# Performance work log

Hardware: AMD Instinct MI355X
Metric: run time of the kernel (lower is better)

The kernel has to match this reference:

```python
import jax, jax.numpy as jnp
import numpy as np
import math

# config constants (match init_kwargs)
N_HEAD = 16
KNN_NUM = 4
MEM_FRAC = 4.0
BOOKKEEPING_FRAC = 0.0
RESID_ONLY = False
RESID_FOUND = 0.5   # set_resid_frac(resid_frac): found/current mix
RESID_CURR = 0.5
KNN_INFLUENCE = 1.0
NEG_INF = jnp.finfo(jnp.float32).min


def setup_inputs() -> dict:
    key = jax.random.key(0)
    k1, k2, k3, k4, k5 = jax.random.split(key, 5)
    B, T, C = 1, 2048, 1024
    H, d = N_HEAD, C // N_HEAD
    M = 8192  # per-head memory-store entries
    return {
        "x": jax.random.normal(k1, (B, T, C), jnp.float32),
        "c_attn_w": jax.random.normal(k2, (3 * C, C), jnp.float32) * 0.02,
        "c_proj_w": jax.random.normal(k3, (C, C), jnp.float32) * 0.02,
        "key_store": jax.random.normal(k4, (H, M, d), jnp.float32),
        "value_store": jax.random.normal(k5, (H, M, d), jnp.float32),
    }


def _knn_get(att, k, q, v, key_store, value_store):
    # att: (B,H,T,T), k/q/v: (B,H,T,d), stores: (H,M,d). B must be 1 (original
    # scatter offset i*t is only consistent for b==1).
    B, H, T, d = k.shape
    scale = 1.0 / math.sqrt(d)
    att_last = att[:, :, -1, :]                     # (B,H,T) last-query column
    # bookkeeping_frac == 0.0 -> skipped; mem_frac truthy -> threshold filter
    mask = att_last >= (1.0 / (MEM_FRAC * T))       # nonzero after zeroing

    # per-head flattened token lists, shape (H, N=B*T, d)
    kh = jnp.swapaxes(k, 0, 1).reshape(H, B * T, d)
    qh = jnp.swapaxes(q, 0, 1).reshape(H, B * T, d)
    vh = jnp.swapaxes(v, 0, 1).reshape(H, B * T, d)
    mask_h = jnp.swapaxes(mask, 0, 1).reshape(H, B * T)

    # exact L2 kNN (FAISS IndexFlatL2 equivalent): d2[h,n,m] = ||kh - ks||^2
    d2 = (jnp.sum(kh * kh, -1)[:, :, None]
          - 2.0 * jnp.einsum('hnd,hmd->hnm', kh, key_store)
          + jnp.sum(key_store * key_store, -1)[:, None, :])
    _, idx = jax.lax.top_k(-d2, KNN_NUM)            # (H,N,K) nearest indices

    h_ix = jnp.arange(H)[:, None, None]
    keys_found = key_store[h_ix, idx]               # (H,N,K,d)
    vals_found = value_store[h_ix, idx]
    keys_found = jnp.moveaxis(keys_found, 2, 0)     # (K,H,N,d)
    vals_found = jnp.moveaxis(vals_found, 2, 0)
    if not RESID_ONLY:
        keys_found = jnp.concatenate([kh[None], keys_found], axis=0)  # (K+1,H,N,d)
        vals_found = jnp.concatenate([vh[None], vals_found], axis=0)

    attf = jnp.einsum('khnd,hnd->khn', keys_found, qh) * scale
    attf = jnp.where(jnp.isnan(attf), NEG_INF, attf)
    attf = jax.nn.softmax(attf * KNN_INFLUENCE, axis=0)
    vals_new = jnp.einsum('khn,khnd->hnd', attf, vals_found)
    if RESID_FOUND > 0 or RESID_CURR > 0:
        vals_new = vals_new * RESID_FOUND + vh * RESID_CURR

    v_out = jnp.where(mask_h[..., None], vals_new, vh)   # scatter-equivalent
    return jnp.swapaxes(v_out.reshape(H, B, T, d), 0, 1)  # (B,H,T,d)


def reference(x, c_attn_w, c_proj_w, key_store, value_store):
    B, T, C = x.shape
    H, d = N_HEAD, C // N_HEAD
    qkv = x @ c_attn_w.T                             # (B,T,3C)
    q, k, v = jnp.split(qkv, 3, axis=2)
    q = jnp.swapaxes(q.reshape(B, T, H, d), 1, 2)    # (B,H,T,d)
    k = jnp.swapaxes(k.reshape(B, T, H, d), 1, 2)
    v = jnp.swapaxes(v.reshape(B, T, H, d), 1, 2)

    att = jnp.einsum('bhqd,bhkd->bhqk', q, k) * (1.0 / math.sqrt(d))
    causal = jnp.tril(jnp.ones((T, T), bool))
    att = jnp.where(causal, att, NEG_INF)
    att = jax.nn.softmax(att, axis=-1)

    # knn_get is @torch.no_grad() in the original -> stop_gradient
    v_new = jax.lax.stop_gradient(
        _knn_get(att, k, q, v, key_store, value_store))

    y = jnp.einsum('bhqk,bhkd->bhqd', att, v_new)
    y = jnp.swapaxes(y, 1, 2).reshape(B, T, C)
    return y @ c_proj_w.T
```

## Files before the change

kernel.cpp:

```cpp
#include <hip/hip_runtime.h>
#include <hip/hip_bf16.h>
#include <math.h>

#define TT 2048
#define CC 1024
#define HH 16
#define DDIM 64
#define MM 8192
#define C3 3072
#define SBIAS 256.0f

typedef __bf16 bf16x8 __attribute__((ext_vector_type(8)));
typedef float f32x4 __attribute__((ext_vector_type(4)));

__device__ __forceinline__ float waveReduceSum(float v) {
#pragma unroll
  for (int off = 32; off > 0; off >>= 1) v += __shfl_xor(v, off, 64);
  return v;
}
__device__ __forceinline__ unsigned umn(unsigned a, unsigned b){ return a<b?a:b; }
__device__ __forceinline__ unsigned umx(unsigned a, unsigned b){ return a>b?a:b; }

__device__ __forceinline__ void gload16(const void* g, void* l) {
  __builtin_amdgcn_global_load_lds(
      (const __attribute__((address_space(1))) unsigned int*)g,
      (__attribute__((address_space(3))) unsigned int*)l, 16, 0, 0);
}

__global__ __launch_bounds__(256) void conv_split_k(const float* __restrict__ src,
    __hip_bfloat16* __restrict__ hi, __hip_bfloat16* __restrict__ lo)
{
  size_t i = (size_t)blockIdx.x*256 + threadIdx.x;
  const float4* p = (const float4*)(src + i*8);
  float4 a = p[0], b = p[1];
  float v[8] = {a.x,a.y,a.z,a.w,b.x,b.y,b.z,b.w};
  bf16x8 H, L;
#pragma unroll
  for (int e = 0; e < 8; ++e) {
    __bf16 hb = (__bf16)v[e];
    H[e] = hb;
    L[e] = (__bf16)(v[e] - (float)hb);
  }
  *reinterpret_cast<bf16x8*>(hi + i*8) = H;
  *reinterpret_cast<bf16x8*>(lo + i*8) = L;
}

__global__ __launch_bounds__(256) void conv_bf16_k(const float* __restrict__ src,
    __hip_bfloat16* __restrict__ dst)
{
  size_t i = (size_t)blockIdx.x*256 + threadIdx.x;
  const float4* p = (const float4*)(src + i*8);
  float4 a = p[0], b = p[1];
  float v[8] = {a.x,a.y,a.z,a.w,b.x,b.y,b.z,b.w};
  bf16x8 H;
#pragma unroll
  for (int e = 0; e < 8; ++e) H[e] = (__bf16)v[e];
  *reinterpret_cast<bf16x8*>(dst + i*8) = H;
}

__global__ __launch_bounds__(256) void conv_ks_k(const float* __restrict__ ks,
    __hip_bfloat16* __restrict__ ksb, float* __restrict__ ksn, float* __restrict__ ksnb)
{
  int row = blockIdx.x*4 + (threadIdx.x>>6);
  int lane = threadIdx.x & 63;
  float v = ks[(size_t)row*64 + lane];
  float sq = waveReduceSum(v*v);
  ksb[(size_t)row*64 + lane] = __float2bfloat16(v);
  if (lane == 0) { ksn[row] = sq; ksnb[row] = sq + SBIAS; }
}

__global__ __launch_bounds__(256) void conv_kb_k(const float* __restrict__ qkv,
    __hip_bfloat16* __restrict__ kb)
{
  int e = blockIdx.x*256 + threadIdx.x;
  int dg = e & 7; int t = (e>>3) & (TT-1); int h = e >> 14;
  const float* src = qkv + (size_t)t*C3 + CC + h*64 + dg*8;
  __hip_bfloat16* dst = kb + ((size_t)(h*TT + t)*64 + dg*8);
#pragma unroll
  for (int i = 0; i < 8; ++i) dst[i] = __float2bfloat16(src[i]);
}

__global__ __launch_bounds__(256) void vtrans_k(const float* __restrict__ vnew,
    __hip_bfloat16* __restrict__ vbT)
{
  __shared__ float tbuf[64][65];
  const int h = blockIdx.y, t0 = blockIdx.x*64, tid = threadIdx.x;
#pragma unroll
  for (int r = 0; r < 16; ++r) {
    int e = r*256 + tid; int row = e>>6, dv = e&63;
    tbuf[row][dv] = vnew[((size_t)h*TT + t0 + row)*64 + dv];
  }
  __syncthreads();
#pragma unroll
  for (int r = 0; r < 16; ++r) {
    int e = r*256 + tid; int dv = e>>6, tt = e&63;
    vbT[((size_t)h*64 + dv)*TT + t0 + tt] = __float2bfloat16(tbuf[tt][dv]);
  }
}

template<bool SPLIT>
__global__ __launch_bounds__(256) void gemm_mfma_k(
    const __hip_bfloat16* __restrict__ Ah, const __hip_bfloat16* __restrict__ Al,
    const __hip_bfloat16* __restrict__ Bh, const __hip_bfloat16* __restrict__ Bl,
    float* __restrict__ Cc, int M, int N, int K)
{
  __shared__ __align__(16) char lds[2][32768];
  const int tid = threadIdx.x;
  const int nbx = N >> 7;
  const int by = blockIdx.x / nbx, bx = blockIdx.x - by*nbx;
  const int m0 = by << 7, n0 = bx << 7;
  const int w = tid >> 6;
  const int l = tid & 63;
  const int wslot = w << 6;
  const int wi = w >> 1, wj = w & 1;
  const int fr = l & 15, fo = l >> 4;
  const int kw = SPLIT ? 32 : 64;
  const int nsteps = K / kw;

  f32x4 acc[4][4];
#pragma unroll
  for (int i = 0; i < 4; ++i)
#pragma unroll
    for (int j = 0; j < 4; ++j) acc[i][j] = f32x4{0.f,0.f,0.f,0.f};

  int srow[4], schg[4];
#pragma unroll
  for (int r = 0; r < 4; ++r) {
    int s = r*256 + tid;
    srow[r] = s >> 3;
    schg[r] = (s & 7) ^ (srow[r] & 7);
  }

  auto stageAB = [&](int buf, int st) {
    const int k0 = st * kw;
#pragma unroll
    for (int r = 0; r < 4; ++r) {
      const __hip_bfloat16 *pa, *pb;
      if (SPLIT) {
        pa = (schg[r] < 4 ? Ah : Al) + (size_t)(m0+srow[r])*K + k0 + (schg[r]&3)*8;
        pb = (schg[r] < 4 ? Bh : Bl) + (size_t)(n0+srow[r])*K + k0 + (schg[r]&3)*8;
      } else {
        pa = Ah + (size_t)(m0+srow[r])*K + k0 + schg[r]*8;
        pb = Bh + (size_t)(n0+srow[r])*K + k0 + schg[r]*8;
      }
      gload16(pa, lds[buf] + (r*256 + wslot)*16);
      gload16(pb, lds[buf] + 16384 + (r*256 + wslot)*16);
    }
  };

  stageAB(0, 0);
  __syncthreads();

  for (int st = 0; st < nsteps; ++st) {
    const int buf = st & 1;
    if (st + 1 < nsteps) stageAB(buf ^ 1, st + 1);
    char* ldsb = lds[buf];

    if (SPLIT) {
      bf16x8 bhf[4], blf[4];
#pragma unroll
      for (int j = 0; j < 4; ++j) {
        int row = wj*64 + j*16 + fr;
        bhf[j] = *(const bf16x8*)(ldsb + 16384 + row*128 + ((fo     ^ (row&7))*16));
        blf[j] = *(const bf16x8*)(ldsb + 16384 + row*128 + (((4+fo) ^ (row&7))*16));
      }
#pragma unroll
      for (int i = 0; i < 4; ++i) {
        int row = wi*64 + i*16 + fr;
        bf16x8 ah = *(const bf16x8*)(ldsb + row*128 + ((fo     ^ (row&7))*16));
        bf16x8 al = *(const bf16x8*)(ldsb + row*128 + (((4+fo) ^ (row&7))*16));
#pragma unroll
        for (int j = 0; j < 4; ++j) {
          acc[i][j] = __builtin_amdgcn_mfma_f32_16x16x32_bf16(al, bhf[j], acc[i][j], 0,0,0);
          acc[i][j] = __builtin_amdgcn_mfma_f32_16x16x32_bf16(ah, blf[j], acc[i][j], 0,0,0);
          acc[i][j] = __builtin_amdgcn_mfma_f32_16x16x32_bf16(ah, bhf[j], acc[i][j], 0,0,0);
        }
      }
    } else {
#pragma unroll
      for (int kk = 0; kk < 2; ++kk) {
        bf16x8 bf[4];
#pragma unroll
        for (int j = 0; j < 4; ++j) {
          int row = wj*64 + j*16 + fr;
          bf[j] = *(const bf16x8*)(ldsb + 16384 + row*128 + (((kk*4+fo) ^ (row&7))*16));
        }
#pragma unroll
        for (int i = 0; i < 4; ++i) {
          int row = wi*64 + i*16 + fr;
          bf16x8 af = *(const bf16x8*)(ldsb + row*128 + (((kk*4+fo) ^ (row&7))*16));
#pragma unroll
          for (int j = 0; j < 4; ++j)
            acc[i][j] = __builtin_amdgcn_mfma_f32_16x16x32_bf16(af, bf[j], acc[i][j], 0,0,0);
        }
      }
    }
    __syncthreads();
  }

  float* ep = (float*)((char*)lds + (size_t)w*8704);
#pragma unroll
  for (int pass = 0; pass < 2; ++pass) {
#pragma unroll
    for (int ii = 0; ii < 2; ++ii) {
      int i = pass*2 + ii;
#pragma unroll
      for (int j = 0; j < 4; ++j)
#pragma unroll
        for (int e = 0; e < 4; ++e)
          ep[(ii*16 + fo*4 + e)*68 + j*16 + fr] = acc[i][j][e];
    }
#pragma unroll
    for (int eidx = 0; eidx < 8; ++eidx) {
      int fi = eidx*64 + l;
      int row = fi >> 4, c4 = fi & 15;
      float4 v4 = *(const float4*)(ep + row*68 + c4*4);
      *(float4*)(Cc + (size_t)(m0 + wi*64 + pass*32 + row)*N + n0 + wj*64 + c4*4) = v4;
    }
  }
}

__global__ __launch_bounds__(256) void attlast_mask_k(const float* __restrict__ qkv, int* __restrict__ mask)
{
  const int h = blockIdx.x;
  __shared__ float ql[64];
  __shared__ float lg[TT];
  __shared__ float red[256];
  const int tid = threadIdx.x;
  if (tid < 64) ql[tid] = qkv[(size_t)(TT-1)*C3 + h*DDIM + tid];
  __syncthreads();
  float lmax = -INFINITY;
  for (int t = tid; t < TT; t += 256) {
    const float* kr = qkv + (size_t)t*C3 + CC + h*DDIM;
    float s = 0.f;
#pragma unroll
    for (int d = 0; d < 64; ++d) s += ql[d] * kr[d];
    s *= 0.125f;
    lg[t] = s;
    lmax = fmaxf(lmax, s);
  }
  red[tid] = lmax; __syncthreads();
  for (int off = 128; off > 0; off >>= 1) { if (tid < off) red[tid] = fmaxf(red[tid], red[tid+off]); __syncthreads(); }
  float mx = red[0];
  __syncthreads();
  float ls = 0.f;
  for (int t = tid; t < TT; t += 256) { float e = expf(lg[t]-mx); lg[t] = e; ls += e; }
  red[tid] = ls; __syncthreads();
  for (int off = 128; off > 0; off >>= 1) { if (tid < off) red[tid] += red[tid+off]; __syncthreads(); }
  float Z = red[0];
  for (int t = tid; t < TT; t += 256) mask[h*TT + t] = (lg[t]/Z >= 1.220703125e-4f) ? 1 : 0;
}

__global__ __launch_bounds__(256) void knn_chunkmin_k(
    const __hip_bfloat16* __restrict__ kb, const __hip_bfloat16* __restrict__ ksb,
    const float* __restrict__ ksnb, unsigned int* __restrict__ cand)
{
  __shared__ __align__(16) char lds[2*8192];
  const int tid = threadIdx.x;
  const int bid = blockIdx.x;
  const int orig = (bid & 7)*64 + (bid >> 3);
  const int h  = orig >> 5;
  const int n0 = (orig & 31) * 64;
  const int w  = tid >> 6;
  const int l  = tid & 63;
  const int cr = l & 15, hi = l >> 4;
  const unsigned crbits = (unsigned)cr << 7;

  bf16x8 af0, af1;
  {
    const __hip_bfloat16* kbh = kb + (size_t)h*TT*64 + (size_t)(n0 + w*16 + cr)*64;
    af0 = *reinterpret_cast<const bf16x8*>(kbh + 0*32 + hi*8);
    af1 = *reinterpret_cast<const bf16x8*>(kbh + 1*32 + hi*8);
  }
  const __hip_bfloat16* ksbh = ksb + (size_t)h*MM*64;
  const float* ksnh = ksnb + (size_t)h*MM;

  const int c0 = tid*2, c1 = tid*2 + 1;
  const int wb0 = (c0>>3)*128 + (((c0&7) ^ ((c0>>3)&7))*16);
  const int wb1 = (c1>>3)*128 + (((c1&7) ^ ((c1>>3)&7))*16);
  const int rb0 = (l&15)*128 + (((0 + hi) ^ (l&7))*16);
  const int rb1 = (l&15)*128 + (((4 + hi) ^ (l&7))*16);

  unsigned cnd[4][4];
#pragma unroll
  for (int i = 0; i < 4; ++i)
#pragma unroll
    for (int c = 0; c < 4; ++c) cnd[i][c] = 0xFFFFFFFFu;

  uint4 r0, r1;
  {
    const uint4* g = reinterpret_cast<const uint4*>(ksbh);
    r0 = g[c0]; r1 = g[c1];
    *reinterpret_cast<uint4*>(lds + wb0) = r0;
    *reinterpret_cast<uint4*>(lds + wb1) = r1;
  }

  for (int tt = 0; tt < 128; ++tt) {
    __syncthreads();
    const int buf = tt & 1;
    char* ldsb = lds + buf*8192;
    if (tt + 1 < 128) {
      const uint4* g = reinterpret_cast<const uint4*>(ksbh + (size_t)(tt+1)*64*64);
      r0 = g[c0]; r1 = g[c1];
    }
    float kn0 = ksnh[tt*64 +  0 + cr];
    float kn1 = ksnh[tt*64 + 16 + cr];
    float kn2 = ksnh[tt*64 + 32 + cr];
    float kn3 = ksnh[tt*64 + 48 + cr];

    f32x4 acc[4];
#pragma unroll
    for (int b = 0; b < 4; ++b) {
      bf16x8 bf0 = *reinterpret_cast<const bf16x8*>(ldsb + b*2048 + rb0);
      bf16x8 bf1 = *reinterpret_cast<const bf16x8*>(ldsb + b*2048 + rb1);
      f32x4 z = {0.f, 0.f, 0.f, 0.f};
      z = __builtin_amdgcn_mfma_f32_16x16x32_bf16(af0, bf0, z, 0, 0, 0);
      z = __builtin_amdgcn_mfma_f32_16x16x32_bf16(af1, bf1, z, 0, 0, 0);
      acc[b] = z;
    }
#pragma unroll
    for (int i = 0; i < 4; ++i) {
      float s0 = fmaf(acc[0][i], -2.f, kn0);
      float s1 = fmaf(acc[1][i], -2.f, kn1);
      float s2 = fmaf(acc[2][i], -2.f, kn2);
      float s3 = fmaf(acc[3][i], -2.f, kn3);
      float m4 = fminf(fminf(s0, s1), fminf(s2, s3));
      unsigned x = (__float_as_uint(m4) & 0xFFFFF800u) | crbits | (unsigned)tt;
      unsigned tmp;
      tmp = umn(cnd[i][0], x); x = umx(cnd[i][0], x); cnd[i][0] = tmp;
      tmp = umn(cnd[i][1], x); x = umx(cnd[i][1], x); cnd[i][1] = tmp;
      tmp = umn(cnd[i][2], x); x = umx(cnd[i][2], x); cnd[i][2] = tmp;
      cnd[i][3] = umn(cnd[i][3], x);
    }
    if (tt + 1 < 128) {
      char* ldsn = lds + (buf^1)*8192;
      *reinterpret_cast<uint4*>(ldsn + wb0) = r0;
      *reinterpret_cast<uint4*>(ldsn + wb1) = r1;
    }
  }

#pragma unroll
  for (int i = 0; i < 4; ++i) {
    int n = n0 + w*16 + hi*4 + i;
    reinterpret_cast<uint4*>(cand)[(size_t)(h*TT + n)*16 + cr] =
        make_uint4(cnd[i][0], cnd[i][1], cnd[i][2], cnd[i][3]);
  }
}

__global__ __launch_bounds__(256) void knn_fused_k(
    const unsigned int* __restrict__ cand, const float* __restrict__ qkv,
    const float* __restrict__ kstore, const float* __restrict__ vstore,
    const float* __restrict__ ksn, const int* __restrict__ mask,
    float* __restrict__ vnew)
{
  const int row = blockIdx.x*4 + (threadIdx.x>>6);
  const int l = threadIdx.x & 63;
  const int h = row >> 11, t = row & (TT-1);
  const float* base = qkv + (size_t)t*C3 + h*64;
  float vh = base[2*CC + l];
  float* outp = vnew + (size_t)row*64;
  if (!mask[row]) { outp[l] = vh; return; }

  unsigned v = cand[(size_t)row*64 + l];
#pragma unroll
  for (int k = 2; k <= 64; k <<= 1)
#pragma unroll
    for (int j = k>>1; j > 0; j >>= 1) {
      unsigned o = __shfl_xor(v, j, 64);
      bool takeMin = ((l & j) == 0) == ((l & k) == 0);
      v = (takeMin == (o < v)) ? o : v;
    }

  const int c = l >> 1;
  const int b = c & 3;
  unsigned vc = __shfl(v, c >> 2, 64);
  const int m = ((int)(vc & 127u))*64 + b*16 + (int)((vc >> 7) & 15u);
  const int p = l & 1;
  {
    const float* kq = base + CC + p*32;
    const float* ksr = kstore + ((size_t)h*MM + m)*64 + p*32;
    float dp = 0.f;
#pragma unroll
    for (int i = 0; i < 8; ++i) {
      float4 a = *(const float4*)(kq + i*4);
      float4 bb = *(const float4*)(ksr + i*4);
      dp = fmaf(a.x,bb.x, fmaf(a.y,bb.y, fmaf(a.z,bb.z, fmaf(a.w,bb.w, dp))));
    }
    dp += __shfl_xor(dp, 1, 64);
    float s = ksn[(size_t)h*MM + m] - 2.f*dp;
    unsigned u = __float_as_uint(s);
    unsigned skey = u ^ (unsigned)(((int)u >> 31) | 0x80000000);
    unsigned khi = (p == 0) ? skey : 0xFFFFFFFFu;
    unsigned klo = (p == 0) ? (unsigned)m : 0xFFFFFFFFu;
#pragma unroll
    for (int k = 2; k <= 64; k <<= 1)
#pragma unroll
      for (int j = k>>1; j > 0; j >>= 1) {
        unsigned oh = __shfl_xor(khi, j, 64);
        unsigned ol = __shfl_xor(klo, j, 64);
        bool takeMin = ((l & j) == 0) == ((l & k) == 0);
        bool oLess = (oh < khi) || (oh == khi && ol < klo);
        if (takeMin == oLess) { khi = oh; klo = ol; }
      }
    v = klo;
  }

  const int m0 = (int)__shfl(v, 0, 64);
  const int m1 = (int)__shfl(v, 1, 64);
  const int m2 = (int)__shfl(v, 2, 64);
  const int m3 = (int)__shfl(v, 3, 64);
  const int g = l >> 3, gl = l & 7;
  float dq = 0.f;
  if (g < 5) {
    int msel = (g == 0) ? m0 : (g == 1) ? m1 : (g == 2) ? m2 : m3;
    const float* qrow = base + gl*8;
    const float* kr = (g < 4) ? (kstore + ((size_t)h*MM + msel)*64 + gl*8)
                              : (base + CC + gl*8);
    float4 a0 = *(const float4*)(qrow);
    float4 a1 = *(const float4*)(qrow + 4);
    float4 b0 = *(const float4*)(kr);
    float4 b1 = *(const float4*)(kr + 4);
    dq = a0.x*b0.x + a0.y*b0.y + a0.z*b0.z + a0.w*b0.w
       + a1.x*b1.x + a1.y*b1.y + a1.z*b1.z + a1.w*b1.w;
  }
  dq += __shfl_xor(dq, 1, 64);
  dq += __shfl_xor(dq, 2, 64);
  dq += __shfl_xor(dq, 4, 64);
  float d0 = __shfl(dq,  0, 64)*0.125f;
  float d1 = __shfl(dq,  8, 64)*0.125f;
  float d2 = __shfl(dq, 16, 64)*0.125f;
  float d3 = __shfl(dq, 24, 64)*0.125f;
  float d4 = __shfl(dq, 32, 64)*0.125f;
  float mx = fmaxf(fmaxf(fmaxf(d0,d1),fmaxf(d2,d3)),d4);
  float w0 = expf(d0-mx), w1 = expf(d1-mx), w2 = expf(d2-mx),
        w3 = expf(d3-mx), w4 = expf(d4-mx);
  float Z = w0+w1+w2+w3+w4;
  float vv = w4*vh
           + w0*vstore[((size_t)h*MM+m0)*64 + l]
           + w1*vstore[((size_t)h*MM+m1)*64 + l]
           + w2*vstore[((size_t)h*MM+m2)*64 + l]
           + w3*vstore[((size_t)h*MM+m3)*64 + l];
  outp[l] = 0.5f*(vv/Z) + 0.5f*vh;
}

__global__ __launch_bounds__(256) void attn_mfma_k(
    const float* __restrict__ qkv, const __hip_bfloat16* __restrict__ kb,
    const __hip_bfloat16* __restrict__ vbT, __hip_bfloat16* __restrict__ yb)
{
  __shared__ __align__(16) char lds[40960];
  const int h = blockIdx.y, bx = blockIdx.x, tid = threadIdx.x;
  const int w = tid>>6, l = tid&63, fr = l&15, fo = l>>4;
  const int wslot = w << 6;
  const __hip_bfloat16* kbh = kb + (size_t)h*TT*64;
  const __hip_bfloat16* vbh = vbT + (size_t)h*64*TT;
  char* Pt = lds + 32768 + w*2048;

  int srow[2], schg[2];
#pragma unroll
  for (int r = 0; r < 2; ++r) {
    int s = r*256 + tid;
    srow[r] = s >> 3;
    schg[r] = (s & 7) ^ (srow[r] & 7);
  }

  auto stageKV = [&](int buf, int kt) {
#pragma unroll
    for (int r = 0; r < 2; ++r) {
      gload16(kbh + (size_t)(kt*64 + srow[r])*64 + schg[r]*8,
              lds + buf*16384 + (r*256 + wslot)*16);
      gload16(vbh + (size_t)srow[r]*TT + kt*64 + schg[r]*8,
              lds + buf*16384 + 8192 + (r*256 + wslot)*16);
    }
  };

  for (int half = 0; half < 2; ++half) {
    const int qblk = half ? (31 - bx) : bx;
    const int q0 = qblk * 64;
    bf16x8 qa[2];
    {
      const float* qrow = qkv + (size_t)(q0 + w*16 + fr)*C3 + h*64;
#pragma unroll
      for (int kk = 0; kk < 2; ++kk) {
        float4 u0 = *(const float4*)(qrow + kk*32 + fo*8);
        float4 u1 = *(const float4*)(qrow + kk*32 + fo*8 + 4);
        bf16x8 t;
        t[0]=(__bf16)u0.x; t[1]=(__bf16)u0.y; t[2]=(__bf16)u0.z; t[3]=(__bf16)u0.w;
        t[4]=(__bf16)u1.x; t[5]=(__bf16)u1.y; t[6]=(__bf16)u1.z; t[7]=(__bf16)u1.w;
        qa[kk] = t;
      }
    }
    float mrow[4], lsum[4];
    f32x4 oacc[4];
#pragma unroll
    for (int e = 0; e < 4; ++e) { mrow[e] = -INFINITY; lsum[e] = 0.f; }
#pragma unroll
    for (int jv = 0; jv < 4; ++jv) oacc[jv] = f32x4{0.f,0.f,0.f,0.f};

    const int ntiles = qblk + 1;
    stageKV(0, 0);
    __syncthreads();

    for (int kt = 0; kt < ntiles; ++kt) {
      const int buf = kt & 1;
      if (kt + 1 < ntiles) stageKV(buf ^ 1, kt + 1);
      char* Kt = lds + buf*16384;
      char* Vt = Kt + 8192;

      f32x4 sv[4];
#pragma unroll
      for (int j = 0; j < 4; ++j) {
        int row = j*16 + fr;
        bf16x8 k0f = *(const bf16x8*)(Kt + row*128 + ((fo     ^ (row&7))*16));
        bf16x8 k1f = *(const bf16x8*)(Kt + row*128 + (((4+fo) ^ (row&7))*16));
        f32x4 z = {0.f,0.f,0.f,0.f};
        z = __builtin_amdgcn_mfma_f32_16x16x32_bf16(qa[0], k0f, z, 0,0,0);
        z = __builtin_amdgcn_mfma_f32_16x16x32_bf16(qa[1], k1f, z, 0,0,0);
        sv[j] = z;
      }
      if (kt == qblk) {
#pragma unroll
        for (int j = 0; j < 4; ++j)
#pragma unroll
          for (int e = 0; e < 4; ++e)
            sv[j][e] = (j*16 + fr <= w*16 + fo*4 + e) ? sv[j][e]*0.125f : -INFINITY;
      } else {
#pragma unroll
        for (int j = 0; j < 4; ++j)
#pragma unroll
          for (int e = 0; e < 4; ++e) sv[j][e] *= 0.125f;
      }
      float rmax[4];
#pragma unroll
      for (int e = 0; e < 4; ++e)
        rmax[e] = fmaxf(fmaxf(sv[0][e], sv[1][e]), fmaxf(sv[2][e], sv[3][e]));
#pragma unroll
      for (int off = 1; off < 16; off <<= 1)
#pragma unroll
        for (int e = 0; e < 4; ++e) rmax[e] = fmaxf(rmax[e], __shfl_xor(rmax[e], off, 64));
      float scl[4];
#pragma unroll
      for (int e = 0; e < 4; ++e) {
        float mn = fmaxf(mrow[e], rmax[e]);
        scl[e] = __expf(mrow[e] - mn);
        mrow[e] = mn;
      }
      float rsum[4] = {0.f,0.f,0.f,0.f};
#pragma unroll
      for (int j = 0; j < 4; ++j) {
        int chunkbase = j*2 + (fr>>3);
        int kvoff = (fr&7)*2;
#pragma unroll
        for (int e = 0; e < 4; ++e) {
          float p = __expf(sv[j][e] - mrow[e]);
          rsum[e] += p;
          int qloc = fo*4 + e;
          *(__bf16*)(Pt + qloc*128 + ((chunkbase ^ (qloc&7))*16) + kvoff) = (__bf16)p;
        }
      }
#pragma unroll
      for (int off = 1; off < 16; off <<= 1)
#pragma unroll
        for (int e = 0; e < 4; ++e) rsum[e] += __shfl_xor(rsum[e], off, 64);
#pragma unroll
      for (int e = 0; e < 4; ++e) lsum[e] = lsum[e]*scl[e] + rsum[e];
#pragma unroll
      for (int jv = 0; jv < 4; ++jv)
#pragma unroll
        for (int e = 0; e < 4; ++e) oacc[jv][e] *= scl[e];

      bf16x8 pa0 = *(const bf16x8*)(Pt + fr*128 + ((fo     ^ (fr&7))*16));
      bf16x8 pa1 = *(const bf16x8*)(Pt + fr*128 + (((4+fo) ^ (fr&7))*16));
#pragma unroll
      for (int jv = 0; jv < 4; ++jv) {
        int row = jv*16 + fr;
        bf16x8 v0f = *(const bf16x8*)(Vt + row*128 + ((fo     ^ (row&7))*16));
        bf16x8 v1f = *(const bf16x8*)(Vt + row*128 + (((4+fo) ^ (row&7))*16));
        oacc[jv] = __builtin_amdgcn_mfma_f32_16x16x32_bf16(pa0, v0f, oacc[jv], 0,0,0);
        oacc[jv] = __builtin_amdgcn_mfma_f32_16x16x32_bf16(pa1, v1f, oacc[jv], 0,0,0);
      }
      __syncthreads();
    }
#pragma unroll
    for (int jv = 0; jv < 4; ++jv)
#pragma unroll
      for (int e = 0; e < 4; ++e) {
        int t = q0 + w*16 + fo*4 + e;
        yb[(size_t)t*CC + h*64 + jv*16 + fr] = __float2bfloat16(oacc[jv][e] / lsum[e]);
      }
  }
}

extern "C" void kernel_launch(void* const* d_in, const int* in_sizes, int n_in,
                              void* d_out, int out_size, void* d_ws, size_t ws_size,
                              hipStream_t stream) {
  const float* x   = (const float*)d_in[0];
  const float* wat = (const float*)d_in[1];
  const float* wpr = (const float*)d_in[2];
  const float* kst = (const float*)d_in[3];
  const float* vst = (const float*)d_in[4];
  float* out = (float*)d_out;

  float* ws    = (float*)d_ws;
  float* qkv   = ws;
  float* ksn   = qkv + (size_t)6291456;
  float* ksnb  = ksn + 131072;
  int*   idxb  = (int*)(ksnb + 131072);
  int*   maskb = idxb + 131072;
  __hip_bfloat16* kb = (__hip_bfloat16*)(maskb + 32768);
  float* candRegion = (float*)kb + 1048576;
  unsigned int* candb = (unsigned int*)candRegion;
  float* vnew = candRegion;
  __hip_bfloat16* vbT = (__hip_bfloat16*)(candRegion + 2097152);
  float* split = candRegion + 2097152 + 1048576;
  __hip_bfloat16* xhi = (__hip_bfloat16*)split;
  __hip_bfloat16* xlo = xhi + 2097152;
  __hip_bfloat16* whi = xlo + 2097152;
  __hip_bfloat16* wlo = whi + 3145728;
  __hip_bfloat16* ksb  = (__hip_bfloat16*)split;
  __hip_bfloat16* wprb = ksb + 8388608;
  __hip_bfloat16* yb   = (__hip_bfloat16*)split;

  conv_split_k<<<dim3(1024), 256, 0, stream>>>(x, xhi, xlo);
  conv_split_k<<<dim3(1536), 256, 0, stream>>>(wat, whi, wlo);
  gemm_mfma_k<true><<<dim3(16*24), 256, 0, stream>>>(xhi, xlo, whi, wlo, qkv, TT, C3, CC);
  conv_kb_k<<<dim3(1024), 256, 0, stream>>>(qkv, kb);
  conv_ks_k<<<dim3(HH*MM/4), 256, 0, stream>>>(kst, ksb, ksn, ksnb);
  conv_bf16_k<<<dim3(512), 256, 0, stream>>>(wpr, wprb);
  attlast_mask_k<<<dim3(HH), 256, 0, stream>>>(qkv, maskb);
  knn_chunkmin_k<<<dim3(512), 256, 0, stream>>>(kb, ksb, ksnb, candb);
  knn_fused_k<<<dim3(HH*TT/4), 256, 0, stream>>>(candb, qkv, kst, vst, ksn, maskb, vnew);
  vtrans_k<<<dim3(32, HH), 256, 0, stream>>>(vnew, vbT);
  attn_mfma_k<<<dim3(16, HH), 256, 0, stream>>>(qkv, kb, vbT, yb);
  gemm_mfma_k<false><<<dim3(16*8), 256, 0, stream>>>(yb, nullptr, wprb, nullptr, out, TT, CC, CC);
}
```

Measured before the change: 314.2 us.

## Fold key norms into MFMA and use async LDS loads with med3 top-4 insertion

The -2 scale is pre-applied to the bf16 key store, and the biased key norm is packed as a bf16 hi/lo pair. A third MFMA against a constant-ones A operand adds that norm into the accumulator, which removes the per-element FMAs in the kNN distance kernel. Key-store tiles are now staged with global_load_lds direct-to-LDS loads instead of register round-trips. The sorted top-4 insertion uses v_med3_u32 in place of min/max chains. The cost is one extra MFMA per block and a slight precision change in the bias term from the bf16 split.

```diff
diff --git a/kernel.cpp b/kernel.cpp
--- a/kernel.cpp
+++ b/kernel.cpp
@@ -20,6 +20,11 @@
 }
 __device__ __forceinline__ unsigned umn(unsigned a, unsigned b){ return a<b?a:b; }
 __device__ __forceinline__ unsigned umx(unsigned a, unsigned b){ return a>b?a:b; }
+__device__ __forceinline__ unsigned umed3(unsigned a, unsigned b, unsigned c){
+  unsigned d;
+  asm("v_med3_u32 %0, %1, %2, %3" : "=v"(d) : "v"(a), "v"(b), "v"(c));
+  return d;
+}
 
 __device__ __forceinline__ void gload16(const void* g, void* l) {
   __builtin_amdgcn_global_load_lds(
@@ -59,14 +64,23 @@
 }
 
 __global__ __launch_bounds__(256) void conv_ks_k(const float* __restrict__ ks,
-    __hip_bfloat16* __restrict__ ksb, float* __restrict__ ksn, float* __restrict__ ksnb)
+    __hip_bfloat16* __restrict__ ksb, float* __restrict__ ksn, unsigned* __restrict__ knhl)
 {
   int row = blockIdx.x*4 + (threadIdx.x>>6);
   int lane = threadIdx.x & 63;
   float v = ks[(size_t)row*64 + lane];
   float sq = waveReduceSum(v*v);
-  ksb[(size_t)row*64 + lane] = __float2bfloat16(v);
-  if (lane == 0) { ksn[row] = sq; ksnb[row] = sq + SBIAS; }
+  ksb[(size_t)row*64 + lane] = __float2bfloat16(-2.f*v);
+  if (lane == 0) {
+    ksn[row] = sq;
+    float b = sq + SBIAS;
+    __hip_bfloat16 hb = __float2bfloat16(b);
+    float hf = __bfloat162float(hb);
+    __hip_bfloat16 lb = __float2bfloat16(b - hf);
+    unsigned h16 = (unsigned)__builtin_bit_cast(unsigned short, hb);
+    unsigned l16 = (unsigned)__builtin_bit_cast(unsigned short, lb);
+    knhl[row] = (l16 << 16) | h16;
+  }
 }
 
 __global__ __launch_bounds__(256) void conv_kb_k(const float* __restrict__ qkv,
@@ -253,7 +267,7 @@
 
 __global__ __launch_bounds__(256) void knn_chunkmin_k(
     const __hip_bfloat16* __restrict__ kb, const __hip_bfloat16* __restrict__ ksb,
-    const float* __restrict__ ksnb, unsigned int* __restrict__ cand)
+    const unsigned* __restrict__ knhl, unsigned int* __restrict__ cand)
 {
   __shared__ __align__(16) char lds[2*8192];
   const int tid = threadIdx.x;
@@ -264,22 +278,26 @@
   const int w  = tid >> 6;
   const int l  = tid & 63;
   const int cr = l & 15, hi = l >> 4;
-  const unsigned crbits = (unsigned)cr << 7;
 
   bf16x8 af0, af1;
   {
     const __hip_bfloat16* kbh = kb + (size_t)h*TT*64 + (size_t)(n0 + w*16 + cr)*64;
-    af0 = *reinterpret_cast<const bf16x8*>(kbh + 0*32 + hi*8);
-    af1 = *reinterpret_cast<const bf16x8*>(kbh + 1*32 + hi*8);
+    af0 = *reinterpret_cast<const bf16x8*>(kbh + hi*8);
+    af1 = *reinterpret_cast<const bf16x8*>(kbh + 32 + hi*8);
+  }
+  bf16x8 aext;
+  {
+    uint4 t = { (l < 16) ? 0x3F803F80u : 0u, 0u, 0u, 0u };
+    aext = __builtin_bit_cast(bf16x8, t);
   }
   const __hip_bfloat16* ksbh = ksb + (size_t)h*MM*64;
-  const float* ksnh = ksnb + (size_t)h*MM;
-
-  const int c0 = tid*2, c1 = tid*2 + 1;
-  const int wb0 = (c0>>3)*128 + (((c0&7) ^ ((c0>>3)&7))*16);
-  const int wb1 = (c1>>3)*128 + (((c1&7) ^ ((c1>>3)&7))*16);
-  const int rb0 = (l&15)*128 + (((0 + hi) ^ (l&7))*16);
-  const int rb1 = (l&15)*128 + (((4 + hi) ^ (l&7))*16);
+  const unsigned* knh = knhl + (size_t)h*MM;
+
+  const int s0 = tid, s1 = tid + 256;
+  const int g0 = (s0 & ~7) | ((s0 & 7) ^ ((s0 >> 3) & 7));
+  const int g1 = (s1 & ~7) | ((s1 & 7) ^ ((s1 >> 3) & 7));
+  const int rb0 = (l&15)*128 + ((hi ^ (l&7))*16);
+  const int rb1 = (l&15)*128 + (((4+hi) ^ (l&7))*16);
 
   unsigned cnd[4][4];
 #pragma unroll
@@ -287,56 +305,45 @@
 #pragma unroll
     for (int c = 0; c < 4; ++c) cnd[i][c] = 0xFFFFFFFFu;
 
-  uint4 r0, r1;
-  {
-    const uint4* g = reinterpret_cast<const uint4*>(ksbh);
-    r0 = g[c0]; r1 = g[c1];
-    *reinterpret_cast<uint4*>(lds + wb0) = r0;
-    *reinterpret_cast<uint4*>(lds + wb1) = r1;
-  }
+  auto stage = [&](int buf, int tt) {
+    const __hip_bfloat16* src = ksbh + (size_t)tt*4096;
+    gload16(src + g0*8, lds + buf*8192 + (w << 10));
+    gload16(src + g1*8, lds + buf*8192 + 4096 + (w << 10));
+  };
+
+  stage(0, 0);
+  __syncthreads();
 
   for (int tt = 0; tt < 128; ++tt) {
-    __syncthreads();
     const int buf = tt & 1;
+    if (tt + 1 < 128) stage(buf ^ 1, tt + 1);
     char* ldsb = lds + buf*8192;
-    if (tt + 1 < 128) {
-      const uint4* g = reinterpret_cast<const uint4*>(ksbh + (size_t)(tt+1)*64*64);
-      r0 = g[c0]; r1 = g[c1];
-    }
-    float kn0 = ksnh[tt*64 +  0 + cr];
-    float kn1 = ksnh[tt*64 + 16 + cr];
-    float kn2 = ksnh[tt*64 + 32 + cr];
-    float kn3 = ksnh[tt*64 + 48 + cr];
+    const unsigned crtt = ((unsigned)cr << 7) | (unsigned)tt;
 
     f32x4 acc[4];
 #pragma unroll
     for (int b = 0; b < 4; ++b) {
+      uint4 kt = { knh[tt*64 + b*16 + cr], 0u, 0u, 0u };
+      bf16x8 bext = __builtin_bit_cast(bf16x8, kt);
       bf16x8 bf0 = *reinterpret_cast<const bf16x8*>(ldsb + b*2048 + rb0);
       bf16x8 bf1 = *reinterpret_cast<const bf16x8*>(ldsb + b*2048 + rb1);
       f32x4 z = {0.f, 0.f, 0.f, 0.f};
+      z = __builtin_amdgcn_mfma_f32_16x16x32_bf16(aext, bext, z, 0, 0, 0);
       z = __builtin_amdgcn_mfma_f32_16x16x32_bf16(af0, bf0, z, 0, 0, 0);
       z = __builtin_amdgcn_mfma_f32_16x16x32_bf16(af1, bf1, z, 0, 0, 0);
       acc[b] = z;
     }
 #pragma unroll
     for (int i = 0; i < 4; ++i) {
-      float s0 = fmaf(acc[0][i], -2.f, kn0);
-      float s1 = fmaf(acc[1][i], -2.f, kn1);
-      float s2 = fmaf(acc[2][i], -2.f, kn2);
-      float s3 = fmaf(acc[3][i], -2.f, kn3);
-      float m4 = fminf(fminf(s0, s1), fminf(s2, s3));
-      unsigned x = (__float_as_uint(m4) & 0xFFFFF800u) | crbits | (unsigned)tt;
-      unsigned tmp;
-      tmp = umn(cnd[i][0], x); x = umx(cnd[i][0], x); cnd[i][0] = tmp;
-      tmp = umn(cnd[i][1], x); x = umx(cnd[i][1], x); cnd[i][1] = tmp;
-      tmp = umn(cnd[i][2], x); x = umx(cnd[i][2], x); cnd[i][2] = tmp;
-      cnd[i][3] = umn(cnd[i][3], x);
-    }
-    if (tt + 1 < 128) {
-      char* ldsn = lds + (buf^1)*8192;
-      *reinterpret_cast<uint4*>(ldsn + wb0) = r0;
-      *reinterpret_cast<uint4*>(ldsn + wb1) = r1;
-    }
+      float m4 = fminf(fminf(fminf(acc[0][i], acc[1][i]), acc[2][i]), acc[3][i]);
+      unsigned x = (__float_as_uint(m4) & 0xFFFFF800u) | crtt;
+      unsigned t0 = umn(cnd[i][0], x);
+      unsigned t1 = umed3(x, cnd[i][0], cnd[i][1]);
+      unsigned t2 = umed3(x, cnd[i][1], cnd[i][2]);
+      unsigned t3 = umed3(x, cnd[i][2], cnd[i][3]);
+      cnd[i][0] = t0; cnd[i][1] = t1; cnd[i][2] = t2; cnd[i][3] = t3;
+    }
+    __syncthreads();
   }
 
 #pragma unroll
@@ -603,8 +610,8 @@
   float* ws    = (float*)d_ws;
   float* qkv   = ws;
   float* ksn   = qkv + (size_t)6291456;
-  float* ksnb  = ksn + 131072;
-  int*   idxb  = (int*)(ksnb + 131072);
+  unsigned* knhl = (unsigned*)(ksn + 131072);
+  int*   idxb  = (int*)(knhl + 131072);
   int*   maskb = idxb + 131072;
   __hip_bfloat16* kb = (__hip_bfloat16*)(maskb + 32768);
   float* candRegion = (float*)kb + 1048576;
@@ -624,10 +631,10 @@
   conv_split_k<<<dim3(1536), 256, 0, stream>>>(wat, whi, wlo);
   gemm_mfma_k<true><<<dim3(16*24), 256, 0, stream>>>(xhi, xlo, whi, wlo, qkv, TT, C3, CC);
   conv_kb_k<<<dim3(1024), 256, 0, stream>>>(qkv, kb);
-  conv_ks_k<<<dim3(HH*MM/4), 256, 0, stream>>>(kst, ksb, ksn, ksnb);
+  conv_ks_k<<<dim3(HH*MM/4), 256, 0, stream>>>(kst, ksb, ksn, knhl);
   conv_bf16_k<<<dim3(512), 256, 0, stream>>>(wpr, wprb);
   attlast_mask_k<<<dim3(HH), 256, 0, stream>>>(qkv, maskb);
-  knn_chunkmin_k<<<dim3(512), 256, 0, stream>>>(kb, ksb, ksnb, candb);
+  knn_chunkmin_k<<<dim3(512), 256, 0, stream>>>(kb, ksb, knhl, candb);
   knn_fused_k<<<dim3(HH*TT/4), 256, 0, stream>>>(candb, qkv, kst, vst, ksn, maskb, vnew);
   vtrans_k<<<dim3(32, HH), 256, 0, stream>>>(vnew, vbT);
   attn_mfma_k<<<dim3(16, HH), 256, 0, stream>>>(qkv, kb, vbT, yb);
```

New measurement: 357.0 us. +13.6%, slower.
